# Performance work log

Measured on AMD Instinct MI355X. Metric: run time of the kernel, lower is better.

Reference implementation:

```python
import jax, jax.numpy as jnp
import numpy as np

N_FFT = 2048
HOP = 512
BATCH = 16
LENGTH = 262144


def _fourier_kernels(n_fft):
    # freq_scale='no': bin k uses frequency k; hann window, fftbins=True
    s = np.arange(n_fft, dtype=np.float64)
    win = 0.5 - 0.5 * np.cos(2.0 * np.pi * s / n_fft)
    phase = 2.0 * np.pi * s[:, None] * s[None, :] / n_fft  # (k, n)
    wsin = (win[None, :] * np.sin(phase)).astype(np.float32)[:, None, :]  # (n_fft,1,n_fft)
    wcos = (win[None, :] * np.cos(phase)).astype(np.float32)[:, None, :]
    return wsin, wcos


def setup_inputs() -> dict:
    key = jax.random.key(0)
    x = jax.random.normal(key, (BATCH, LENGTH), dtype=jnp.float32)
    wsin_np, wcos_np = _fourier_kernels(N_FFT)
    return {"x": x, "wsin": jnp.asarray(wsin_np), "wcos": jnp.asarray(wcos_np)}


def reference(x, wsin, wcos):
    # broadcast (batch, len) -> (batch, 1, len)
    x = x[:, None, :]
    # center=True, pad_mode='reflect': pad n_fft//2 on both sides
    x = jnp.pad(x, ((0, 0), (0, 0), (N_FFT // 2, N_FFT // 2)), mode="reflect")
    dn = ("NCH", "OIH", "NCH")
    imag = jax.lax.conv_general_dilated(x, wsin, (HOP,), "VALID", dimension_numbers=dn)
    real = jax.lax.conv_general_dilated(x, wcos, (HOP,), "VALID", dimension_numbers=dn)
    return (real, -imag)  # each (batch, n_fft, frames)
```

## Files before the change

### kernel.cpp

```cpp
#include <hip/hip_runtime.h>
#include <stdint.h>
#include <math.h>


#define N_FFT   2048
#define HOP     512
#define BATCH   16
#define LENGTH  262144
#define FRAMES  513
#define OHALF   ((size_t)BATCH * N_FFT * FRAMES)
#define KS      1026
#define PAIRS   257

#define WIDX(w) ((w) + ((w) >> 4))
#define LDSN    2176

__device__ __forceinline__ float2 cmul(float2 a, float2 w) {
    return make_float2(a.x * w.x - a.y * w.y, a.x * w.y + a.y * w.x);
}


__global__ void init_tables(float2* __restrict__ tw, float* __restrict__ win) {
    int i = blockIdx.x * 256 + threadIdx.x;
    if (i < 2048) {
        double a = -2.0 * M_PI * (double)i / 2048.0;
        tw[i] = make_float2((float)cos(a), (float)sin(a));
        double aw = 2.0 * M_PI * (double)i / 2048.0;
        win[i] = (float)(0.5 - 0.5 * cos(aw));
    }
}

__global__ __launch_bounds__(256) void fft_pairs(
    const float* __restrict__ x, const float2* __restrict__ tw,
    const float* __restrict__ win, float2* __restrict__ sc)
{
    __shared__ float2 buf[2][LDSN];

    const int tid = threadIdx.x;
    const int p   = blockIdx.x;
    const int b   = blockIdx.y;
    const int fA  = 2 * p;
    const int fB  = 2 * p + 1;
    const bool hasB = (fB < FRAMES);
    const float* xb = x + (size_t)b * LENGTH;

    if (p >= 1 && p <= 254) {
        const float4* xA = (const float4*)(xb + fA * HOP - (N_FFT / 2));
        const float4* xB = (const float4*)(xb + fB * HOP - (N_FFT / 2));
        const float4* w4 = (const float4*)win;
        #pragma unroll
        for (int j = 0; j < 2; ++j) {
            int q = tid + 256 * j;
            float4 wv = w4[q];
            float4 va = xA[q];
            float4 vb = xB[q];
            int wn = 4 * q + (q >> 2);
            buf[0][wn + 0] = make_float2(va.x * wv.x, vb.x * wv.x);
            buf[0][wn + 1] = make_float2(va.y * wv.y, vb.y * wv.y);
            buf[0][wn + 2] = make_float2(va.z * wv.z, vb.z * wv.z);
            buf[0][wn + 3] = make_float2(va.w * wv.w, vb.w * wv.w);
        }
    } else {
        #pragma unroll
        for (int j = 0; j < 8; ++j) {
            int n = tid + 256 * j;
            float w = win[n];
            int ja = fA * HOP + n - (N_FFT / 2);
            ja = (ja < 0) ? -ja : ((ja >= LENGTH) ? 2 * LENGTH - 2 - ja : ja);
            float va = xb[ja] * w;
            float vb = 0.f;
            if (hasB) {
                int jb = fB * HOP + n - (N_FFT / 2);
                jb = (jb < 0) ? -jb : ((jb >= LENGTH) ? 2 * LENGTH - 2 - jb : jb);
                vb = xb[jb] * w;
            }
            buf[0][WIDX(n)] = make_float2(va, vb);
        }
    }
    __syncthreads();

    int src = 0;
    #pragma unroll
    for (int ls = 0; ls < 5; ++ls) {
        const int s  = 1 << (2 * ls);
        const int os = s + (s >> 4);
        const float2* X = buf[src];
        float2*       Y = buf[src ^ 1];
        #pragma unroll
        for (int u = 0; u < 2; ++u) {
            int idx = tid + 256 * u;
            int sp  = idx & ~(s - 1);
            int wi  = WIDX(idx);
            float2 a0 = X[wi];
            float2 a1 = X[wi + 544];
            float2 a2 = X[wi + 1088];
            float2 a3 = X[wi + 1632];
            float2 t0 = make_float2(a0.x + a2.x, a0.y + a2.y);
            float2 t1 = make_float2(a0.x - a2.x, a0.y - a2.y);
            float2 t2 = make_float2(a1.x + a3.x, a1.y + a3.y);
            float2 t3 = make_float2(a1.x - a3.x, a1.y - a3.y);
            float2 y0 = make_float2(t0.x + t2.x, t0.y + t2.y);
            float2 y1 = make_float2(t1.x + t3.y, t1.y - t3.x);
            float2 y2 = make_float2(t0.x - t2.x, t0.y - t2.y);
            float2 y3 = make_float2(t1.x - t3.y, t1.y + t3.x);
            float2 w1 = tw[sp];
            float2 w2 = tw[2 * sp];
            float2 w3 = tw[3 * sp];
            int wo = WIDX(idx + 3 * sp);
            Y[wo]          = y0;
            Y[wo + os]     = cmul(y1, w1);
            Y[wo + 2 * os] = cmul(y2, w2);
            Y[wo + 3 * os] = cmul(y3, w3);
        }
        __syncthreads();
        src ^= 1;
    }

    const float2* X5 = buf[src];
    float2* scA = sc + ((size_t)b * FRAMES + fA) * KS;
    float2* scB = sc + ((size_t)b * FRAMES + fB) * KS;
    #pragma unroll
    for (int j = 0; j < 5; ++j) {
        int k = tid + 256 * j;
        if (k <= 1024) {
            int m2 = (2048 - k) & 2047;
            float2 u0, u1, v0, v1;
            if (k < 1024) {
                int wa = WIDX(k);
                u0 = X5[wa]; u1 = X5[wa + 1088];
                u0 = make_float2(u0.x + u1.x, u0.y + u1.y);
            } else {
                u0 = X5[0]; u1 = X5[1088];
                u0 = make_float2(u0.x - u1.x, u0.y - u1.y);
            }
            if (m2 < 1024) {
                int wa = WIDX(m2);
                v0 = X5[wa]; v1 = X5[wa + 1088];
                v0 = make_float2(v0.x + v1.x, v0.y + v1.y);
            } else {
                int wa = WIDX(m2 - 1024);
                v0 = X5[wa]; v1 = X5[wa + 1088];
                v0 = make_float2(v0.x - v1.x, v0.y - v1.y);
            }
            float2 A = make_float2(0.5f * (u0.x + v0.x), 0.5f * (u0.y - v0.y));
            float2 B = make_float2(0.5f * (u0.y + v0.y), 0.5f * (v0.x - u0.x));
            scA[k] = A;
            if (hasB) scB[k] = B;
        }
    }
}

__global__ __launch_bounds__(256) void transpose_out(
    const float2* __restrict__ sc, float* __restrict__ out)
{
    __shared__ float tre[64][65];
    __shared__ float tim[64][65];

    const int b  = blockIdx.x;
    const int kt = blockIdx.y;
    const int ft = blockIdx.z;
    const int k0 = kt * 64;
    const int f0 = ft * 64;
    const int tid = threadIdx.x;

    #pragma unroll
    for (int i = 0; i < 16; ++i) {
        int idx = tid + 256 * i;
        int fl = idx >> 6, kl = idx & 63;
        int f = f0 + fl, k = k0 + kl;
        float2 v = make_float2(0.f, 0.f);
        if (f < FRAMES && k <= 1024)
            v = sc[((size_t)b * FRAMES + f) * KS + k];
        tre[fl][kl] = v.x;
        tim[fl][kl] = v.y;
    }
    __syncthreads();

    const int wave = tid >> 6, lane = tid & 63;
    const int t = f0 + lane;
    const bool tok = (t < FRAMES);
    float* o0 = out + (size_t)b * ((size_t)N_FFT * FRAMES);
    float* o1 = out + OHALF + (size_t)b * ((size_t)N_FFT * FRAMES);

    for (int kl = wave; kl < 64; kl += 4) {
        int k = k0 + kl;
        if (k > 1024) continue;
        float vr = tre[lane][kl];
        float vi = tim[lane][kl];
        if (tok) {
            o0[(size_t)k * FRAMES + t] = vr;
            o1[(size_t)k * FRAMES + t] = vi;
            if (k >= 1 && k <= 1023) {
                o0[(size_t)(N_FFT - k) * FRAMES + t] = vr;
                o1[(size_t)(N_FFT - k) * FRAMES + t] = -vi;
            }
        }
    }
}


__global__ void dft_naive(const float* __restrict__ x,
                          const float* __restrict__ wsin,
                          const float* __restrict__ wcos,
                          float* __restrict__ out)
{
    size_t i = (size_t)blockIdx.x * 256 + threadIdx.x;
    if (i >= OHALF) return;
    int t = (int)(i % FRAMES);
    size_t r = i / FRAMES;
    int k = (int)(r % N_FFT);
    int b = (int)(r / N_FFT);
    float sr = 0.f, si = 0.f;
    int base = t * HOP - N_FFT / 2;
    for (int n = 0; n < N_FFT; ++n) {
        int j = base + n;
        j = (j < 0) ? -j : ((j >= LENGTH) ? (2 * LENGTH - 2 - j) : j);
        float xv = x[(size_t)b * LENGTH + j];
        sr += xv * wcos[(size_t)k * N_FFT + n];
        si += xv * wsin[(size_t)k * N_FFT + n];
    }
    out[i] = sr;
    out[OHALF + i] = -si;
}


extern "C" void kernel_launch(void* const* d_in, const int* in_sizes, int n_in,
                              void* d_out, int out_size, void* d_ws, size_t ws_size,
                              hipStream_t stream) {
    const float* x    = (const float*)d_in[0];
    const float* wsin = (const float*)d_in[1];
    const float* wcos = (const float*)d_in[2];
    float* out = (float*)d_out;

    const size_t sc_f2   = (size_t)BATCH * FRAMES * KS;
    const size_t need_ft = 24576 + sc_f2 * sizeof(float2);
    if (ws_size >= need_ft) {
        float2* tw  = (float2*)d_ws;
        float*  win = (float*)((char*)d_ws + 16384);
        float2* sc  = (float2*)((char*)d_ws + 24576);
        init_tables<<<8, 256, 0, stream>>>(tw, win);
        fft_pairs<<<dim3(PAIRS, BATCH), 256, 0, stream>>>(x, tw, win, sc);
        transpose_out<<<dim3(BATCH, 17, 9), 256, 0, stream>>>(sc, out);
        return;
    }

    dft_naive<<<(int)((OHALF + 255) / 256), 256, 0, stream>>>(x, wsin, wcos, out);
}
```

Measured before the change: 252.9 us.

## Fuse first radix-4 stage into load, compute twiddles and window inline

```diff
diff --git a/kernel.cpp b/kernel.cpp
--- a/kernel.cpp
+++ b/kernel.cpp
@@ -15,24 +15,18 @@
 #define WIDX(w) ((w) + ((w) >> 4))
 #define LDSN    2176
 
+#define TWO_PI_OVER_N  3.0679615757712823e-3f
+
 __device__ __forceinline__ float2 cmul(float2 a, float2 w) {
     return make_float2(a.x * w.x - a.y * w.y, a.x * w.y + a.y * w.x);
 }
-
-
-__global__ void init_tables(float2* __restrict__ tw, float* __restrict__ win) {
-    int i = blockIdx.x * 256 + threadIdx.x;
-    if (i < 2048) {
-        double a = -2.0 * M_PI * (double)i / 2048.0;
-        tw[i] = make_float2((float)cos(a), (float)sin(a));
-        double aw = 2.0 * M_PI * (double)i / 2048.0;
-        win[i] = (float)(0.5 - 0.5 * cos(aw));
-    }
-}
+__device__ __forceinline__ float2 csq(float2 w) {
+    return make_float2(w.x * w.x - w.y * w.y, 2.f * w.x * w.y);
+}
+
 
 __global__ __launch_bounds__(256) void fft_pairs(
-    const float* __restrict__ x, const float2* __restrict__ tw,
-    const float* __restrict__ win, float2* __restrict__ sc)
+    const float* __restrict__ x, float2* __restrict__ sc)
 {
     __shared__ float2 buf[2][LDSN];
 
@@ -43,45 +37,80 @@
     const int fB  = 2 * p + 1;
     const bool hasB = (fB < FRAMES);
     const float* xb = x + (size_t)b * LENGTH;
-
-    if (p >= 1 && p <= 254) {
-        const float4* xA = (const float4*)(xb + fA * HOP - (N_FFT / 2));
-        const float4* xB = (const float4*)(xb + fB * HOP - (N_FFT / 2));
-        const float4* w4 = (const float4*)win;
+    const bool interior = (p >= 1 && p <= 254);
+
+    {
+        const int baseA = fA * HOP - (N_FFT / 2);
+        const int baseB = fB * HOP - (N_FFT / 2);
         #pragma unroll
-        for (int j = 0; j < 2; ++j) {
-            int q = tid + 256 * j;
-            float4 wv = w4[q];
-            float4 va = xA[q];
-            float4 vb = xB[q];
-            int wn = 4 * q + (q >> 2);
-            buf[0][wn + 0] = make_float2(va.x * wv.x, vb.x * wv.x);
-            buf[0][wn + 1] = make_float2(va.y * wv.y, vb.y * wv.y);
-            buf[0][wn + 2] = make_float2(va.z * wv.z, vb.z * wv.z);
-            buf[0][wn + 3] = make_float2(va.w * wv.w, vb.w * wv.w);
-        }
-    } else {
-        #pragma unroll
-        for (int j = 0; j < 8; ++j) {
-            int n = tid + 256 * j;
-            float w = win[n];
-            int ja = fA * HOP + n - (N_FFT / 2);
-            ja = (ja < 0) ? -ja : ((ja >= LENGTH) ? 2 * LENGTH - 2 - ja : ja);
-            float va = xb[ja] * w;
-            float vb = 0.f;
-            if (hasB) {
-                int jb = fB * HOP + n - (N_FFT / 2);
-                jb = (jb < 0) ? -jb : ((jb >= LENGTH) ? 2 * LENGTH - 2 - jb : jb);
-                vb = xb[jb] * w;
-            }
-            buf[0][WIDX(n)] = make_float2(va, vb);
+        for (int u = 0; u < 2; ++u) {
+            int idx = tid + 256 * u;
+            float sn, cs;
+            __sincosf((float)idx * TWO_PI_OVER_N, &sn, &cs);
+            float w0 = 0.5f - 0.5f * cs;
+            float w1v = 0.5f + 0.5f * sn;
+            float w2v = 0.5f + 0.5f * cs;
+            float w3v = 0.5f - 0.5f * sn;
+
+            float xa0, xa1, xa2, xa3, xb0, xb1, xb2, xb3;
+            if (interior) {
+                xa0 = xb[baseA + idx];
+                xa1 = xb[baseA + idx + 512];
+                xa2 = xb[baseA + idx + 1024];
+                xa3 = xb[baseA + idx + 1536];
+                xb0 = xb[baseB + idx];
+                xb1 = xb[baseB + idx + 512];
+                xb2 = xb[baseB + idx + 1024];
+                xb3 = xb[baseB + idx + 1536];
+            } else {
+                #pragma unroll
+                for (int m = 0; m < 4; ++m) {
+                    int ja = baseA + idx + 512 * m;
+                    ja = (ja < 0) ? -ja : ((ja >= LENGTH) ? 2 * LENGTH - 2 - ja : ja);
+                    float va = xb[ja];
+                    float vb = 0.f;
+                    if (hasB) {
+                        int jb = baseB + idx + 512 * m;
+                        jb = (jb < 0) ? -jb : ((jb >= LENGTH) ? 2 * LENGTH - 2 - jb : jb);
+                        vb = xb[jb];
+                    }
+                    if (m == 0) { xa0 = va; xb0 = vb; }
+                    else if (m == 1) { xa1 = va; xb1 = vb; }
+                    else if (m == 2) { xa2 = va; xb2 = vb; }
+                    else { xa3 = va; xb3 = vb; }
+                }
+            }
+
+            float2 a0 = make_float2(xa0 * w0, xb0 * w0);
+            float2 a1 = make_float2(xa1 * w1v, xb1 * w1v);
+            float2 a2 = make_float2(xa2 * w2v, xb2 * w2v);
+            float2 a3 = make_float2(xa3 * w3v, xb3 * w3v);
+
+            float2 t0 = make_float2(a0.x + a2.x, a0.y + a2.y);
+            float2 t1 = make_float2(a0.x - a2.x, a0.y - a2.y);
+            float2 t2 = make_float2(a1.x + a3.x, a1.y + a3.y);
+            float2 t3 = make_float2(a1.x - a3.x, a1.y - a3.y);
+            float2 y0 = make_float2(t0.x + t2.x, t0.y + t2.y);
+            float2 y1 = make_float2(t1.x + t3.y, t1.y - t3.x);
+            float2 y2 = make_float2(t0.x - t2.x, t0.y - t2.y);
+            float2 y3 = make_float2(t1.x - t3.y, t1.y + t3.x);
+
+            float2 tw1 = make_float2(cs, -sn);
+            float2 tw2 = csq(tw1);
+            float2 tw3 = cmul(tw1, tw2);
+
+            int wo = WIDX(4 * idx);
+            buf[0][wo]     = y0;
+            buf[0][wo + 1] = cmul(y1, tw1);
+            buf[0][wo + 2] = cmul(y2, tw2);
+            buf[0][wo + 3] = cmul(y3, tw3);
         }
     }
     __syncthreads();
 
     int src = 0;
     #pragma unroll
-    for (int ls = 0; ls < 5; ++ls) {
+    for (int ls = 1; ls < 5; ++ls) {
         const int s  = 1 << (2 * ls);
         const int os = s + (s >> 4);
         const float2* X = buf[src];
@@ -95,6 +124,13 @@
             float2 a1 = X[wi + 544];
             float2 a2 = X[wi + 1088];
             float2 a3 = X[wi + 1632];
+
+            float sn, cs;
+            __sincosf((float)sp * TWO_PI_OVER_N, &sn, &cs);
+            float2 w1 = make_float2(cs, -sn);
+            float2 w2 = csq(w1);
+            float2 w3 = cmul(w1, w2);
+
             float2 t0 = make_float2(a0.x + a2.x, a0.y + a2.y);
             float2 t1 = make_float2(a0.x - a2.x, a0.y - a2.y);
             float2 t2 = make_float2(a1.x + a3.x, a1.y + a3.y);
@@ -103,9 +139,7 @@
             float2 y1 = make_float2(t1.x + t3.y, t1.y - t3.x);
             float2 y2 = make_float2(t0.x - t2.x, t0.y - t2.y);
             float2 y3 = make_float2(t1.x - t3.y, t1.y + t3.x);
-            float2 w1 = tw[sp];
-            float2 w2 = tw[2 * sp];
-            float2 w3 = tw[3 * sp];
+
             int wo = WIDX(idx + 3 * sp);
             Y[wo]          = y0;
             Y[wo + os]     = cmul(y1, w1);
@@ -233,13 +267,10 @@
     float* out = (float*)d_out;
 
     const size_t sc_f2   = (size_t)BATCH * FRAMES * KS;
-    const size_t need_ft = 24576 + sc_f2 * sizeof(float2);
+    const size_t need_ft = sc_f2 * sizeof(float2);
     if (ws_size >= need_ft) {
-        float2* tw  = (float2*)d_ws;
-        float*  win = (float*)((char*)d_ws + 16384);
-        float2* sc  = (float2*)((char*)d_ws + 24576);
-        init_tables<<<8, 256, 0, stream>>>(tw, win);
-        fft_pairs<<<dim3(PAIRS, BATCH), 256, 0, stream>>>(x, tw, win, sc);
+        float2* sc = (float2*)d_ws;
+        fft_pairs<<<dim3(PAIRS, BATCH), 256, 0, stream>>>(x, sc);
         transpose_out<<<dim3(BATCH, 17, 9), 256, 0, stream>>>(sc, out);
         return;
     }
```

Result: faster. 245.4 us (-2.9%).
